# Kernel tuning notes

Hardware: AMD Instinct MI355X
Metric: run time of the kernel (lower is better)

## Reference

```python
import jax, jax.numpy as jnp
import numpy as np

EPS_BN = 1e-5
NEG = -9e15


def _bn_train(x, g, b):
    # x: [B, C, N]; training-mode BatchNorm1d with batch stats (biased var)
    m = jnp.mean(x, axis=(0, 2), keepdims=True)
    v = jnp.mean((x - m) ** 2, axis=(0, 2), keepdims=True)
    return (x - m) * jax.lax.rsqrt(v + EPS_BN) * g[None, :, None] + b[None, :, None]


def _conv1x1(w, x, b=None):
    # w: [O, C], x: [B, C, N] -> [B, O, N]
    y = jnp.einsum('oc,bcn->bon', w, x)
    if b is not None:
        y = y + b[None, :, None]
    return y


def _sa_layer(x, maskb, qk_w, v_w, v_b, t_w, t_b, bn_g, bn_b):
    # x: [B, C, N], maskb: [B, N] bool
    q = jnp.einsum('hc,bcn->bhn', qk_w, x)          # shared q/k weights
    energy = jnp.einsum('bhn,bhm->bnm', q, q)        # [B, N, N]
    pair = maskb[:, :, None] & maskb[:, None, :]
    energy = jnp.where(pair, energy, NEG)
    attn = jax.nn.softmax(energy, axis=-1)
    attn = attn / (1e-9 + jnp.sum(attn, axis=1, keepdims=True))  # L1 renorm over dim=1
    x_v = _conv1x1(v_w, x, v_b)                      # [B, C, N]
    x_r = jnp.einsum('bcn,bnm->bcm', x_v, attn)      # bmm(x_v, attention)
    t = _conv1x1(t_w, x - x_r, t_b)
    x_r = jax.nn.relu(_bn_train(t, bn_g, bn_b))
    return x + x_r


def setup_inputs() -> dict:
    key = jax.random.key(0)
    ks = jax.random.split(key, 16)
    B, C, N = 16, 256, 2048
    H = C // 4
    s = 0.05
    inp = {
        'x': jax.random.normal(ks[0], (B, C, N), jnp.float32),
        'mask': jax.random.randint(ks[1], (B, N), 0, 2, jnp.int32),
        'conv1_w': jax.random.normal(ks[2], (C, C), jnp.float32) * s,
        'conv2_w': jax.random.normal(ks[3], (C, C), jnp.float32) * s,
        'bn1_g': jnp.ones((C,), jnp.float32),
        'bn1_b': jnp.zeros((C,), jnp.float32),
        'bn2_g': jnp.ones((C,), jnp.float32),
        'bn2_b': jnp.zeros((C,), jnp.float32),
        'sa_qk_w': jax.random.normal(ks[4], (4, H, C), jnp.float32) * s,
        'sa_v_w': jax.random.normal(ks[5], (4, C, C), jnp.float32) * s,
        'sa_v_b': jax.random.normal(ks[6], (4, C), jnp.float32) * s,
        'sa_t_w': jax.random.normal(ks[7], (4, C, C), jnp.float32) * s,
        'sa_t_b': jax.random.normal(ks[8], (4, C), jnp.float32) * s,
        'sa_bn_g': jnp.ones((4, C), jnp.float32),
        'sa_bn_b': jnp.zeros((4, C), jnp.float32),
    }
    return inp


def reference(x, mask, conv1_w, conv2_w, bn1_g, bn1_b, bn2_g, bn2_b,
              sa_qk_w, sa_v_w, sa_v_b, sa_t_w, sa_t_b, sa_bn_g, sa_bn_b):
    maskb = mask.astype(bool)
    x = jax.nn.relu(_bn_train(_conv1x1(conv1_w, x), bn1_g, bn1_b))
    x = jax.nn.relu(_bn_train(_conv1x1(conv2_w, x), bn2_g, bn2_b))
    outs = []
    for i in range(4):
        x = _sa_layer(x, maskb, sa_qk_w[i], sa_v_w[i], sa_v_b[i],
                      sa_t_w[i], sa_t_b[i], sa_bn_g[i], sa_bn_b[i])
        outs.append(x)
    return jnp.concatenate(outs, axis=1)  # [B, 4C, N]
```

## Files before the change

kernel.cpp:

```cpp
#include <hip/hip_runtime.h>
#include <math.h>

#define BB 16
#define CC 256
#define NN 2048
#define HH 64
#define ATTSC 4096.0f
#define ATTINV (1.0f/4096.0f)
#define SQRTL2E 1.2011224087864498f
#define NEGB (-1.0e30f)
#define POSB (1.0e30f)

typedef _Float16 f16x8 __attribute__((ext_vector_type(8)));
typedef float f32x4 __attribute__((ext_vector_type(4)));

__device__ __forceinline__ f32x4 mfma16(f16x8 a, f16x8 b, f32x4 c) {
  return __builtin_amdgcn_mfma_f32_16x16x32_f16(a, b, c, 0, 0, 0);
}
__device__ __forceinline__ unsigned short f2h(float f) {
  _Float16 h = (_Float16)f;
  return __builtin_bit_cast(unsigned short, h);
}
__device__ __forceinline__ float h2f(unsigned short u) {
  return (float)__builtin_bit_cast(_Float16, u);
}
__device__ __forceinline__ unsigned pkrtz(float a, float b) {
  auto h = __builtin_amdgcn_cvt_pkrtz(a, b);
  return __builtin_bit_cast(unsigned, h);
}
__device__ __forceinline__ unsigned short* sp(unsigned short* base, int row, int colh) {
  return (unsigned short*)((char*)base + (row << 7) + (((colh << 1)) ^ ((row & 7) << 4)));
}
__device__ __forceinline__ const unsigned short* spc(const unsigned short* base, int row, int colh) {
  return (const unsigned short*)((const char*)base + (row << 7) + (((colh << 1)) ^ ((row & 7) << 4)));
}

__global__ __launch_bounds__(256)
void castw_kernel(const float* __restrict__ in, unsigned short* __restrict__ out,
                  int n, float scale)
{
  const int i = blockIdx.x*256 + threadIdx.x;
  if (i < n) out[i] = f2h(in[i]*scale);
}

__global__ __launch_bounds__(256)
void tcast_kernel(const float* __restrict__ src, long sstride,
                  unsigned short* __restrict__ dst)
{
  const int b = blockIdx.z, n0 = blockIdx.x*64, c0 = blockIdx.y*64;
  const int t = threadIdx.x;
  __shared__ float tile[64][66];
  const float* sb = src + (long)b*sstride;
  #pragma unroll
  for (int p = 0; p < 4; p++) {
    const int cr = (t>>4) + p*16;
    const int nq = (t&15)*4;
    const float4 v = *(const float4*)&sb[(long)(c0+cr)*NN + n0 + nq];
    tile[cr][nq+0] = v.x; tile[cr][nq+1] = v.y;
    tile[cr][nq+2] = v.z; tile[cr][nq+3] = v.w;
  }
  __syncthreads();
  unsigned short* db = dst + (long)b*NN*CC;
  #pragma unroll
  for (int p = 0; p < 4; p++) {
    const int nr = (t>>4) + p*16;
    const int cq = (t&15)*4;
    ushort4 o;
    o.x = f2h(tile[cq+0][nr]); o.y = f2h(tile[cq+1][nr]);
    o.z = f2h(tile[cq+2][nr]); o.w = f2h(tile[cq+3][nr]);
    *(ushort4*)&db[(long)(n0+nr)*CC + c0 + cq] = o;
  }
}

__global__ __launch_bounds__(256)
void gemm_xw_kernel(const unsigned short* __restrict__ A,
                    const unsigned short* __restrict__ W,
                    const float* __restrict__ bias,
                    unsigned short* __restrict__ out, int ocols)
{
  const int n0 = blockIdx.x*64, o0 = blockIdx.y*64, b = blockIdx.z;
  const int t = threadIdx.x;
  const int w = t >> 6, l = t & 63, lr = l & 15, lg = l >> 4;
  const int wr = w >> 1, wc = w & 1;
  __shared__ unsigned short Al[64][72];
  __shared__ unsigned short Bl[64][72];
  const unsigned short* Ab = A + ((long)b*NN + n0)*CC;
  const int srow = t >> 3, sg = t & 7;
  f32x4 acc[2][2];
  #pragma unroll
  for (int i = 0; i < 2; i++)
    #pragma unroll
    for (int j = 0; j < 2; j++) acc[i][j] = f32x4{0.f,0.f,0.f,0.f};

  for (int kt = 0; kt < 4; kt++) {
    const int k0 = kt*64;
    const uint4 a0 = *(const uint4*)&Ab[(long)srow*CC + k0 + sg*8];
    const uint4 a1 = *(const uint4*)&Ab[(long)(srow+32)*CC + k0 + sg*8];
    const uint4 w0 = *(const uint4*)&W[(long)(o0+srow)*CC + k0 + sg*8];
    const uint4 w1 = *(const uint4*)&W[(long)(o0+srow+32)*CC + k0 + sg*8];
    __syncthreads();
    *(uint4*)&Al[srow][sg*8] = a0;  *(uint4*)&Al[srow+32][sg*8] = a1;
    *(uint4*)&Bl[srow][sg*8] = w0;  *(uint4*)&Bl[srow+32][sg*8] = w1;
    __syncthreads();
    #pragma unroll
    for (int kf = 0; kf < 2; kf++) {
      f16x8 af0 = *(const f16x8*)&Al[wr*32 + lr]     [kf*32 + lg*8];
      f16x8 af1 = *(const f16x8*)&Al[wr*32 + 16 + lr][kf*32 + lg*8];
      f16x8 bf0 = *(const f16x8*)&Bl[wc*32 + lr]     [kf*32 + lg*8];
      f16x8 bf1 = *(const f16x8*)&Bl[wc*32 + 16 + lr][kf*32 + lg*8];
      acc[0][0] = mfma16(af0, bf0, acc[0][0]);
      acc[0][1] = mfma16(af0, bf1, acc[0][1]);
      acc[1][0] = mfma16(af1, bf0, acc[1][0]);
      acc[1][1] = mfma16(af1, bf1, acc[1][1]);
    }
  }
  #pragma unroll
  for (int j = 0; j < 2; j++) {
    const int oc = o0 + wc*32 + j*16 + lr;
    const float bo = bias ? bias[oc] : 0.f;
    #pragma unroll
    for (int i = 0; i < 2; i++) {
      const int nb = n0 + wr*32 + i*16 + lg*4;
      #pragma unroll
      for (int r = 0; r < 4; r++)
        out[((long)b*NN + nb + r)*ocols + oc] = f2h(acc[i][j][r] + bo);
    }
  }
}

__global__ __launch_bounds__(256)
void gemm_dxw_kernel(const unsigned short* __restrict__ X,
                     const unsigned short* __restrict__ XR,
                     const float* __restrict__ csumv,
                     const unsigned short* __restrict__ W,
                     const float* __restrict__ bias,
                     unsigned short* __restrict__ out)
{
  const int n0 = blockIdx.x*64, o0 = blockIdx.y*64, b = blockIdx.z;
  const int t = threadIdx.x;
  const int w = t >> 6, l = t & 63, lr = l & 15, lg = l >> 4;
  const int wr = w >> 1, wc = w & 1;
  __shared__ unsigned short Al[64][72];
  __shared__ unsigned short Bl[64][72];
  const unsigned short* Xb  = X  + ((long)b*NN + n0)*CC;
  const unsigned short* XRb = XR + ((long)b*NN + n0)*CC;
  const int srow = t >> 3, sg = t & 7;
  const long nrow0 = (long)b*NN + n0 + srow;
  const float inv0 = 1.f/(1e-9f + csumv[nrow0]);
  const float inv1 = 1.f/(1e-9f + csumv[nrow0+32]);
  f32x4 acc[2][2];
  #pragma unroll
  for (int i = 0; i < 2; i++)
    #pragma unroll
    for (int j = 0; j < 2; j++) acc[i][j] = f32x4{0.f,0.f,0.f,0.f};

  for (int kt = 0; kt < 4; kt++) {
    const int k0 = kt*64;
    const uint4 xa  = *(const uint4*)&Xb [(long)srow*CC + k0 + sg*8];
    const uint4 xra = *(const uint4*)&XRb[(long)srow*CC + k0 + sg*8];
    const uint4 xb_ = *(const uint4*)&Xb [(long)(srow+32)*CC + k0 + sg*8];
    const uint4 xrb = *(const uint4*)&XRb[(long)(srow+32)*CC + k0 + sg*8];
    const uint4 w0 = *(const uint4*)&W[(long)(o0+srow)*CC + k0 + sg*8];
    const uint4 w1 = *(const uint4*)&W[(long)(o0+srow+32)*CC + k0 + sg*8];
    uint4 da, db_;
    {
      const unsigned short* xs = (const unsigned short*)&xa;
      const unsigned short* rs = (const unsigned short*)&xra;
      unsigned short* ds = (unsigned short*)&da;
      #pragma unroll
      for (int j = 0; j < 8; j++) ds[j] = f2h(h2f(xs[j]) - h2f(rs[j])*inv0);
      xs = (const unsigned short*)&xb_;
      rs = (const unsigned short*)&xrb;
      ds = (unsigned short*)&db_;
      #pragma unroll
      for (int j = 0; j < 8; j++) ds[j] = f2h(h2f(xs[j]) - h2f(rs[j])*inv1);
    }
    __syncthreads();
    *(uint4*)&Al[srow][sg*8] = da;  *(uint4*)&Al[srow+32][sg*8] = db_;
    *(uint4*)&Bl[srow][sg*8] = w0;  *(uint4*)&Bl[srow+32][sg*8] = w1;
    __syncthreads();
    #pragma unroll
    for (int kf = 0; kf < 2; kf++) {
      f16x8 af0 = *(const f16x8*)&Al[wr*32 + lr]     [kf*32 + lg*8];
      f16x8 af1 = *(const f16x8*)&Al[wr*32 + 16 + lr][kf*32 + lg*8];
      f16x8 bf0 = *(const f16x8*)&Bl[wc*32 + lr]     [kf*32 + lg*8];
      f16x8 bf1 = *(const f16x8*)&Bl[wc*32 + 16 + lr][kf*32 + lg*8];
      acc[0][0] = mfma16(af0, bf0, acc[0][0]);
      acc[0][1] = mfma16(af0, bf1, acc[0][1]);
      acc[1][0] = mfma16(af1, bf0, acc[1][0]);
      acc[1][1] = mfma16(af1, bf1, acc[1][1]);
    }
  }
  #pragma unroll
  for (int j = 0; j < 2; j++) {
    const int oc = o0 + wc*32 + j*16 + lr;
    const float bo = bias[oc];
    #pragma unroll
    for (int i = 0; i < 2; i++) {
      const int nb = n0 + wr*32 + i*16 + lg*4;
      #pragma unroll
      for (int r = 0; r < 4; r++)
        out[((long)b*NN + nb + r)*CC + oc] = f2h(acc[i][j][r] + bo);
    }
  }
}

__global__ __launch_bounds__(256)
void gemm_wx_kernel(const unsigned short* __restrict__ W,
                    const unsigned short* __restrict__ X,
                    const float* __restrict__ bias,
                    unsigned short* __restrict__ out)
{
  const int n0 = blockIdx.x*64, o0 = blockIdx.y*64, b = blockIdx.z;
  const int t = threadIdx.x;
  const int w = t >> 6, l = t & 63, lr = l & 15, lg = l >> 4;
  const int wr = w >> 1, wc = w & 1;
  __shared__ unsigned short Al[64][72];
  __shared__ unsigned short Bl[64][72];
  const unsigned short* Xb = X + ((long)b*NN + n0)*CC;
  const int srow = t >> 3, sg = t & 7;
  f32x4 acc[2][2];
  #pragma unroll
  for (int i = 0; i < 2; i++)
    #pragma unroll
    for (int j = 0; j < 2; j++) acc[i][j] = f32x4{0.f,0.f,0.f,0.f};

  for (int kt = 0; kt < 4; kt++) {
    const int k0 = kt*64;
    const uint4 w0 = *(const uint4*)&W[(long)(o0+srow)*CC + k0 + sg*8];
    const uint4 w1 = *(const uint4*)&W[(long)(o0+srow+32)*CC + k0 + sg*8];
    const uint4 x0 = *(const uint4*)&Xb[(long)srow*CC + k0 + sg*8];
    const uint4 x1 = *(const uint4*)&Xb[(long)(srow+32)*CC + k0 + sg*8];
    __syncthreads();
    *(uint4*)&Al[srow][sg*8] = w0;  *(uint4*)&Al[srow+32][sg*8] = w1;
    *(uint4*)&Bl[srow][sg*8] = x0;  *(uint4*)&Bl[srow+32][sg*8] = x1;
    __syncthreads();
    #pragma unroll
    for (int kf = 0; kf < 2; kf++) {
      f16x8 af0 = *(const f16x8*)&Al[wr*32 + lr]     [kf*32 + lg*8];
      f16x8 af1 = *(const f16x8*)&Al[wr*32 + 16 + lr][kf*32 + lg*8];
      f16x8 bf0 = *(const f16x8*)&Bl[wc*32 + lr]     [kf*32 + lg*8];
      f16x8 bf1 = *(const f16x8*)&Bl[wc*32 + 16 + lr][kf*32 + lg*8];
      acc[0][0] = mfma16(af0, bf0, acc[0][0]);
      acc[0][1] = mfma16(af0, bf1, acc[0][1]);
      acc[1][0] = mfma16(af1, bf0, acc[1][0]);
      acc[1][1] = mfma16(af1, bf1, acc[1][1]);
    }
  }
  #pragma unroll
  for (int j = 0; j < 2; j++) {
    const int nc = n0 + wc*32 + j*16 + lr;
    #pragma unroll
    for (int i = 0; i < 2; i++) {
      #pragma unroll
      for (int r = 0; r < 4; r++) {
        const int oc = o0 + wr*32 + i*16 + lg*4 + r;
        out[((long)b*CC + oc)*NN + nc] = f2h(acc[i][j][r] + bias[oc]);
      }
    }
  }
}

__global__ __launch_bounds__(256)
void rowstat_kernel(const unsigned short* __restrict__ qT, const int* __restrict__ mask,
                    float* __restrict__ rmax, float* __restrict__ rinv)
{
  const int b = blockIdx.y, n0 = blockIdx.x*64;
  const int t = threadIdx.x, w = t>>6, l = t&63, lr = l&15, lg = l>>4;
  __shared__ unsigned short qs[64*64];
  __shared__ int ml[64];
  const int srow = t>>3, sg = t&7;
  const unsigned short* qbase = qT + (long)b*NN*HH;
  *(uint4*)sp(qs, srow,    sg*8) = *(const uint4*)&qbase[(long)(n0+srow)*HH + sg*8];
  *(uint4*)sp(qs, srow+32, sg*8) = *(const uint4*)&qbase[(long)(n0+srow+32)*HH + sg*8];
  int maskn[4];
  #pragma unroll
  for (int r = 0; r < 4; r++) maskn[r] = mask[(long)b*NN + n0 + w*16 + lg*4 + r];
  __syncthreads();
  f16x8 af0 = *(const f16x8*)spc(qs, w*16 + lr, lg*8);
  f16x8 af1 = *(const f16x8*)spc(qs, w*16 + lr, 32 + lg*8);
  float mx[4], sm[4];
  #pragma unroll
  for (int r = 0; r < 4; r++) { mx[r] = -INFINITY; sm[r] = 0.f; }

  for (int m0 = 0; m0 < NN; m0 += 64) {
    __syncthreads();
    *(uint4*)sp(qs, srow,    sg*8) = *(const uint4*)&qbase[(long)(m0+srow)*HH + sg*8];
    *(uint4*)sp(qs, srow+32, sg*8) = *(const uint4*)&qbase[(long)(m0+srow+32)*HH + sg*8];
    if (t < 64) ml[t] = mask[(long)b*NN + m0 + t];
    __syncthreads();
    float sv[4][4];
    #pragma unroll
    for (int tm = 0; tm < 4; tm++) {
      f32x4 s = f32x4{0.f,0.f,0.f,0.f};
      s = mfma16(af0, *(const f16x8*)spc(qs, tm*16 + lr, lg*8),      s);
      s = mfma16(af1, *(const f16x8*)spc(qs, tm*16 + lr, 32 + lg*8), s);
      const int cm = ml[tm*16 + lr];
      #pragma unroll
      for (int r = 0; r < 4; r++) sv[tm][r] = (maskn[r] && cm) ? s[r] : NEGB;
    }
    #pragma unroll
    for (int r = 0; r < 4; r++) {
      const float tmx = fmaxf(fmaxf(sv[0][r], sv[1][r]), fmaxf(sv[2][r], sv[3][r]));
      const float nm  = fmaxf(mx[r], tmx);
      sm[r] = sm[r]*exp2f(mx[r]-nm)
            + exp2f(sv[0][r]-nm) + exp2f(sv[1][r]-nm)
            + exp2f(sv[2][r]-nm) + exp2f(sv[3][r]-nm);
      mx[r] = nm;
    }
  }
  #pragma unroll
  for (int off = 1; off < 16; off <<= 1) {
    #pragma unroll
    for (int r = 0; r < 4; r++) {
      const float om = __shfl_xor(mx[r], off, 64);
      const float os = __shfl_xor(sm[r], off, 64);
      const float nm = fmaxf(mx[r], om);
      sm[r] = sm[r]*exp2f(mx[r]-nm) + os*exp2f(om-nm);
      mx[r] = nm;
    }
  }
  if (lr == 0) {
    #pragma unroll
    for (int r = 0; r < 4; r++) {
      const long idx = (long)b*NN + n0 + w*16 + lg*4 + r;
      rmax[idx] = maskn[r] ? mx[r] : POSB;
      rinv[idx] = 1.f/sm[r];
    }
  }
}

__global__ __launch_bounds__(256)
void yatt_kernel(const unsigned short* __restrict__ qT, const unsigned short* __restrict__ xv,
                 const int* __restrict__ mask, const float* __restrict__ rmax,
                 const float* __restrict__ rinv, unsigned short* __restrict__ xrTh,
                 float* __restrict__ csum)
{
  const int bid = blockIdx.x;
  const int swz = (bid & 7)*64 + (bid >> 3);
  const int b  = swz >> 5;
  const int m0 = (swz & 31) * 64;
  const int t = threadIdx.x, w = t>>6, l = t&63, lr = l&15, lg = l>>4;

  __shared__ unsigned short qm[64*64];
  __shared__ unsigned short qn[64*64];
  __shared__ unsigned short at[64*64];
  __shared__ float csred[4][4][16];

  const unsigned short* qbase = qT + (long)b*NN*HH;
  const unsigned short* xvb = xv + (long)b*CC*NN;
  const int srow = t>>3, sg = t&7;

  *(uint4*)sp(qm, srow,    sg*8) = *(const uint4*)&qbase[(long)(m0+srow)*HH + sg*8];
  *(uint4*)sp(qm, srow+32, sg*8) = *(const uint4*)&qbase[(long)(m0+srow+32)*HH + sg*8];
  float mcf[4];
  #pragma unroll
  for (int tm = 0; tm < 4; tm++)
    mcf[tm] = mask[(long)b*NN + m0 + tm*16 + lr] ? 1.f : 0.f;

  f32x4 acc[4][4];
  #pragma unroll
  for (int mi = 0; mi < 4; mi++)
    #pragma unroll
    for (int ci = 0; ci < 4; ci++) acc[mi][ci] = f32x4{0.f,0.f,0.f,0.f};
  float cs[4] = {0.f, 0.f, 0.f, 0.f};
  const int nb = w*16 + lg*4;

  for (int nc = 0; nc < NN; nc += 64) {
    __syncthreads();
    *(uint4*)sp(qn, srow,    sg*8) = *(const uint4*)&qbase[(long)(nc+srow)*HH + sg*8];
    *(uint4*)sp(qn, srow+32, sg*8) = *(const uint4*)&qbase[(long)(nc+srow+32)*HH + sg*8];
    const float4 rm4 = *(const float4*)&rmax[(long)b*NN + nc + nb];
    const float4 ri4 = *(const float4*)&rinv[(long)b*NN + nc + nb];
    const int4   mn4 = *(const int4*)&mask[(long)b*NN + nc + nb];
    f16x8 xb0[4], xb1[4];
    #pragma unroll
    for (int ci = 0; ci < 4; ci++) {
      const unsigned short* xp = &xvb[(long)(w*64 + ci*16 + lr)*NN + nc];
      xb0[ci] = *(const f16x8*)(xp + lg*8);
      xb1[ci] = *(const f16x8*)(xp + 32 + lg*8);
    }
    __syncthreads();
    const float rmv[4] = {rm4.x, rm4.y, rm4.z, rm4.w};
    const float rvs[4] = {ri4.x*ATTSC, ri4.y*ATTSC, ri4.z*ATTSC, ri4.w*ATTSC};
    const float dsc[4] = {mn4.x ? 0.f : rvs[0], mn4.y ? 0.f : rvs[1],
                          mn4.z ? 0.f : rvs[2], mn4.w ? 0.f : rvs[3]};
    const f16x8 a0 = *(const f16x8*)spc(qn, w*16 + lr, lg*8);
    const f16x8 a1 = *(const f16x8*)spc(qn, w*16 + lr, 32 + lg*8);
    #pragma unroll
    for (int tm = 0; tm < 4; tm++) {
      const f16x8 bq0 = *(const f16x8*)spc(qm, tm*16 + lr, lg*8);
      const f16x8 bq1 = *(const f16x8*)spc(qm, tm*16 + lr, 32 + lg*8);
      f32x4 s = mfma16(a0, bq0, f32x4{0.f,0.f,0.f,0.f});
      s = mfma16(a1, bq1, s);
      const float c0 = rvs[0]*mcf[tm], c1 = rvs[1]*mcf[tm];
      const float c2 = rvs[2]*mcf[tm], c3 = rvs[3]*mcf[tm];
      const float a0_ = exp2f(s[0]-rmv[0])*c0 + dsc[0];
      const float a1_ = exp2f(s[1]-rmv[1])*c1 + dsc[1];
      const float a2_ = exp2f(s[2]-rmv[2])*c2 + dsc[2];
      const float a3_ = exp2f(s[3]-rmv[3])*c3 + dsc[3];
      cs[tm] += (a0_ + a1_) + (a2_ + a3_);
      uint2 pk;
      pk.x = pkrtz(a0_, a1_);
      pk.y = pkrtz(a2_, a3_);
      *(uint2*)sp(at, tm*16 + lr, nb) = pk;
    }
    __syncthreads();
    #pragma unroll
    for (int mi = 0; mi < 4; mi++) {
      const f16x8 aa0 = *(const f16x8*)spc(at, mi*16 + lr, lg*8);
      const f16x8 aa1 = *(const f16x8*)spc(at, mi*16 + lr, 32 + lg*8);
      #pragma unroll
      for (int ci = 0; ci < 4; ci++) {
        acc[mi][ci] = mfma16(aa0, xb0[ci], acc[mi][ci]);
        acc[mi][ci] = mfma16(aa1, xb1[ci], acc[mi][ci]);
      }
    }
  }

  #pragma unroll
  for (int mi = 0; mi < 4; mi++)
    #pragma unroll
    for (int ci = 0; ci < 4; ci++)
      #pragma unroll
      for (int r = 0; r < 4; r++)
        xrTh[((long)b*NN + m0 + mi*16 + lg*4 + r)*CC + w*64 + ci*16 + lr] =
            f2h(acc[mi][ci][r] * ATTINV);

  #pragma unroll
  for (int tm = 0; tm < 4; tm++) {
    cs[tm] += __shfl_xor(cs[tm], 16, 64);
    cs[tm] += __shfl_xor(cs[tm], 32, 64);
    if (lg == 0) csred[tm][w][lr] = cs[tm];
  }
  __syncthreads();
  if (t < 64) {
    const int tm = t >> 4, mr = t & 15;
    const float v = csred[tm][0][mr] + csred[tm][1][mr]
                  + csred[tm][2][mr] + csred[tm][3][mr];
    csum[(long)b*NN + m0 + tm*16 + mr] = v * ATTINV;
  }
}

__global__ __launch_bounds__(256)
void bnstatsA_kernel(const unsigned short* __restrict__ tTh, float* __restrict__ part)
{
  const int k = blockIdx.x;
  const int c = threadIdx.x;
  float s = 0.f, sq = 0.f;
  const long r0 = (long)k*128;
  for (int r = 0; r < 128; r++) {
    const float v = h2f(tTh[(r0 + r)*CC + c]);
    s += v; sq += v*v;
  }
  part[(long)k*CC + c] = s;
  part[(long)(256 + k)*CC + c] = sq;
}

__global__ __launch_bounds__(1024)
void bnstatsB_kernel(const float* __restrict__ part,
                     float* __restrict__ mean, float* __restrict__ istd)
{
  const int t = threadIdx.x, c = t & 255, q = t >> 8;
  float s = 0.f, sq = 0.f;
  for (int k = q*64; k < q*64 + 64; k++) {
    s  += part[(long)k*CC + c];
    sq += part[(long)(256 + k)*CC + c];
  }
  __shared__ float ls[4][256], lq[4][256];
  ls[q][c] = s; lq[q][c] = sq;
  __syncthreads();
  if (q == 0) {
    s  = ls[0][c] + ls[1][c] + ls[2][c] + ls[3][c];
    sq = lq[0][c] + lq[1][c] + lq[2][c] + lq[3][c];
    const float mu = s / (float)(BB*NN);
    mean[c] = mu;
    istd[c] = rsqrtf(sq/(float)(BB*NN) - mu*mu + 1e-5f);
  }
}

__global__ __launch_bounds__(256)
void bnapplyA_kernel(const unsigned short* __restrict__ tTh, const float* __restrict__ mean,
                     const float* __restrict__ istd, const float* __restrict__ g,
                     const float* __restrict__ bt, unsigned short* __restrict__ xTo)
{
  __shared__ float sc[CC], sh[CC];
  const int t = threadIdx.x;
  {
    const float is = istd[t], gg = g[t];
    sc[t] = is*gg; sh[t] = bt[t] - mean[t]*is*gg;
  }
  __syncthreads();
  const long i = (long)blockIdx.x*256 + t;
  const long base = i*8;
  const int c8 = (int)(base & 255);
  const uint4 v = *(const uint4*)&tTh[base];
  const unsigned short* hs = (const unsigned short*)&v;
  uint4 ou;
  unsigned short* os = (unsigned short*)&ou;
  #pragma unroll
  for (int j = 0; j < 8; j++)
    os[j] = f2h(fmaxf(h2f(hs[j])*sc[c8+j] + sh[c8+j], 0.f));
  *(uint4*)&xTo[base] = ou;
}

__global__ __launch_bounds__(256)
void bnfuse_kernel(const unsigned short* __restrict__ tTh, const float* __restrict__ mean,
                   const float* __restrict__ istd, const float* __restrict__ g,
                   const float* __restrict__ bt, const float* __restrict__ resid,
                   long rstride, float* __restrict__ outp, long ostride,
                   unsigned short* __restrict__ xtn)
{
  const int b = blockIdx.z, n0 = blockIdx.x*64, c0 = blockIdx.y*64;
  const int t = threadIdx.x;
  __shared__ float tile[64][66];
  const unsigned short* tb_ = tTh + ((long)b*NN + n0)*CC;
  const int cq = (t&15)*4;
  float scv[4], shv[4];
  #pragma unroll
  for (int j = 0; j < 4; j++) {
    const int c = c0 + cq + j;
    const float is = istd[c], gg = g[c];
    scv[j] = is*gg; shv[j] = bt[c] - mean[c]*is*gg;
  }
  #pragma unroll
  for (int p = 0; p < 4; p++) {
    const int nr = (t>>4) + p*16;
    const ushort4 v = *(const ushort4*)&tb_[(long)nr*CC + c0 + cq];
    tile[cq+0][nr] = fmaxf(h2f(v.x)*scv[0] + shv[0], 0.f);
    tile[cq+1][nr] = fmaxf(h2f(v.y)*scv[1] + shv[1], 0.f);
    tile[cq+2][nr] = fmaxf(h2f(v.z)*scv[2] + shv[2], 0.f);
    tile[cq+3][nr] = fmaxf(h2f(v.w)*scv[3] + shv[3], 0.f);
  }
  __syncthreads();
  const int nq = (t&15)*4;
  #pragma unroll
  for (int p = 0; p < 4; p++) {
    const int cr = (t>>4) + p*16;
    float4 o;
    o.x = tile[cr][nq+0]; o.y = tile[cr][nq+1];
    o.z = tile[cr][nq+2]; o.w = tile[cr][nq+3];
    if (resid) {
      const float4 rv = *(const float4*)&resid[(long)b*rstride + (long)(c0+cr)*NN + n0 + nq];
      o.x += rv.x; o.y += rv.y; o.z += rv.z; o.w += rv.w;
    }
    *(float4*)&outp[(long)b*ostride + (long)(c0+cr)*NN + n0 + nq] = o;
    tile[cr][nq+0] = o.x; tile[cr][nq+1] = o.y;
    tile[cr][nq+2] = o.z; tile[cr][nq+3] = o.w;
  }
  if (xtn) {
    __syncthreads();
    #pragma unroll
    for (int p = 0; p < 4; p++) {
      const int nr = (t>>4) + p*16;
      ushort4 o;
      o.x = f2h(tile[cq+0][nr]); o.y = f2h(tile[cq+1][nr]);
      o.z = f2h(tile[cq+2][nr]); o.w = f2h(tile[cq+3][nr]);
      *(ushort4*)&xtn[((long)b*NN + n0+nr)*CC + c0 + cq] = o;
    }
  }
}

extern "C" void kernel_launch(void* const* d_in, const int* in_sizes, int n_in,
                              void* d_out, int out_size, void* d_ws, size_t ws_size,
                              hipStream_t stream)
{
  const float* x_in   = (const float*)d_in[0];
  const int*   mask   = (const int*)d_in[1];
  const float* conv1w = (const float*)d_in[2];
  const float* conv2w = (const float*)d_in[3];
  const float* bn1g   = (const float*)d_in[4];
  const float* bn1b   = (const float*)d_in[5];
  const float* bn2g   = (const float*)d_in[6];
  const float* bn2b   = (const float*)d_in[7];
  const float* qkw    = (const float*)d_in[8];
  const float* vw     = (const float*)d_in[9];
  const float* vb     = (const float*)d_in[10];
  const float* tw     = (const float*)d_in[11];
  const float* tb     = (const float*)d_in[12];
  const float* bng    = (const float*)d_in[13];
  const float* bnb    = (const float*)d_in[14];
  float* out = (float*)d_out;

  const long BCN = (long)BB*CC*NN;
  const long CN  = (long)CC*NN;
  const long BN  = (long)BB*NN;
  char* p = (char*)d_ws;
  unsigned short* xTa  = (unsigned short*)p; p += BCN*2;
  unsigned short* xTb  = (unsigned short*)p; p += BCN*2;
  unsigned short* qTb  = (unsigned short*)p; p += (long)BB*NN*HH*2;
  unsigned short* xvb  = (unsigned short*)p; p += BCN*2;
  unsigned short* tTh  = (unsigned short*)p; p += BCN*2;
  unsigned short* xrTh = (unsigned short*)p; p += BCN*2;
  float* xbuf  = (float*)p; p += BCN*4;
  float* rmaxb = (float*)p; p += BN*4;
  float* rinvb = (float*)p; p += BN*4;
  float* csumb = (float*)p; p += BN*4;
  float* partb = (float*)p; p += 512L*CC*4;
  float* meanb = (float*)p; p += CC*4;
  float* istdb = (float*)p; p += CC*4;
  unsigned short* wc1 = (unsigned short*)p; p += (long)CC*CC*2;
  unsigned short* wc2 = (unsigned short*)p; p += (long)CC*CC*2;
  unsigned short* wqk = (unsigned short*)p; p += 4L*HH*CC*2;
  unsigned short* wv  = (unsigned short*)p; p += 4L*CC*CC*2;
  unsigned short* wt  = (unsigned short*)p; p += 4L*CC*CC*2;

  const dim3 gT(NN/64, CC/64, BB);
  const dim3 gQ(NN/64, 1, BB);
  const dim3 gRS(NN/64, BB);
  const dim3 blk(256);

  castw_kernel<<<dim3(256), blk, 0, stream>>>(conv1w, wc1, CC*CC, 1.f);
  castw_kernel<<<dim3(256), blk, 0, stream>>>(conv2w, wc2, CC*CC, 1.f);
  castw_kernel<<<dim3(256), blk, 0, stream>>>(qkw, wqk, 4*HH*CC, SQRTL2E);
  castw_kernel<<<dim3(1024), blk, 0, stream>>>(vw, wv, 4*CC*CC, 1.f);
  castw_kernel<<<dim3(1024), blk, 0, stream>>>(tw, wt, 4*CC*CC, 1.f);

  tcast_kernel<<<gT, blk, 0, stream>>>(x_in, CN, xTa);
  gemm_xw_kernel<<<gT, blk, 0, stream>>>(xTa, wc1, nullptr, tTh, CC);
  bnstatsA_kernel<<<dim3(256), blk, 0, stream>>>(tTh, partb);
  bnstatsB_kernel<<<dim3(1), dim3(1024), 0, stream>>>(partb, meanb, istdb);
  bnapplyA_kernel<<<dim3(4096), blk, 0, stream>>>(tTh, meanb, istdb, bn1g, bn1b, xTb);
  gemm_xw_kernel<<<gT, blk, 0, stream>>>(xTb, wc2, nullptr, tTh, CC);
  bnstatsA_kernel<<<dim3(256), blk, 0, stream>>>(tTh, partb);
  bnstatsB_kernel<<<dim3(1), dim3(1024), 0, stream>>>(partb, meanb, istdb);
  bnfuse_kernel<<<gT, blk, 0, stream>>>(tTh, meanb, istdb, bn2g, bn2b,
                                        nullptr, 0, xbuf, CN, xTa);

  unsigned short* cur = xTa;
  unsigned short* nxt = xTb;
  for (int i = 0; i < 4; i++) {
    gemm_xw_kernel<<<gQ, blk, 0, stream>>>(cur, wqk + (long)i*HH*CC, nullptr, qTb, HH);
    rowstat_kernel<<<gRS, blk, 0, stream>>>(qTb, mask, rmaxb, rinvb);
    gemm_wx_kernel<<<gT, blk, 0, stream>>>(wv + (long)i*CC*CC, cur, vb + (long)i*CC, xvb);
    yatt_kernel<<<dim3(512), blk, 0, stream>>>(qTb, xvb, mask, rmaxb, rinvb, xrTh, csumb);
    gemm_dxw_kernel<<<gT, blk, 0, stream>>>(cur, xrTh, csumb,
                                            wt + (long)i*CC*CC, tb + (long)i*CC, tTh);
    bnstatsA_kernel<<<dim3(256), blk, 0, stream>>>(tTh, partb);
    bnstatsB_kernel<<<dim3(1), dim3(1024), 0, stream>>>(partb, meanb, istdb);
    const float* resid = (i == 0) ? xbuf : (out + (long)(i-1)*CN);
    const long rstr = (i == 0) ? CN : 4*CN;
    bnfuse_kernel<<<gT, blk, 0, stream>>>(tTh, meanb, istdb,
                                          bng + (long)i*CC, bnb + (long)i*CC,
                                          resid, rstr, out + (long)i*CN, 4*CN,
                                          (i < 3) ? nxt : nullptr);
    unsigned short* tmp = cur; cur = nxt; nxt = tmp;
  }

  (void)in_sizes; (void)n_in; (void)out_size; (void)ws_size;
}
```

Baseline: 802.4 us.

## Widen attention kernel to 512 threads and 128-wide key chunks

The fused attention-times-values kernel now runs with 8 waves per block and processes 128 key columns per iteration instead of 64. Each wave covers 32 output channels instead of 64, which halves its accumulator registers, and the number of loop iterations and barriers is halved. The attention tile in shared memory doubles to 128 columns with a new swizzle helper. The goal is more waves in flight for latency hiding and fewer barriers, at the cost of more shared memory per block and redundant exp computation per 128-column chunk.

```diff
diff --git a/kernel.cpp b/kernel.cpp
--- a/kernel.cpp
+++ b/kernel.cpp
@@ -33,6 +33,12 @@
 }
 __device__ __forceinline__ const unsigned short* spc(const unsigned short* base, int row, int colh) {
   return (const unsigned short*)((const char*)base + (row << 7) + (((colh << 1)) ^ ((row & 7) << 4)));
+}
+__device__ __forceinline__ unsigned short* sp2(unsigned short* base, int row, int colh) {
+  return (unsigned short*)((char*)base + (row << 8) + (((colh << 1)) ^ ((row & 7) << 4)));
+}
+__device__ __forceinline__ const unsigned short* spc2(const unsigned short* base, int row, int colh) {
+  return (const unsigned short*)((const char*)base + (row << 8) + (((colh << 1)) ^ ((row & 7) << 4)));
 }
 
 __global__ __launch_bounds__(256)
@@ -330,7 +336,7 @@
   }
 }
 
-__global__ __launch_bounds__(256)
+__global__ __launch_bounds__(512)
 void yatt_kernel(const unsigned short* __restrict__ qT, const unsigned short* __restrict__ xv,
                  const int* __restrict__ mask, const float* __restrict__ rmax,
                  const float* __restrict__ rinv, unsigned short* __restrict__ xrTh,
@@ -343,42 +349,42 @@
   const int t = threadIdx.x, w = t>>6, l = t&63, lr = l&15, lg = l>>4;
 
   __shared__ unsigned short qm[64*64];
-  __shared__ unsigned short qn[64*64];
-  __shared__ unsigned short at[64*64];
-  __shared__ float csred[4][4][16];
+  __shared__ unsigned short qn[128*64];
+  __shared__ unsigned short at[64*128];
+  __shared__ float csred[4][8][16];
 
   const unsigned short* qbase = qT + (long)b*NN*HH;
   const unsigned short* xvb = xv + (long)b*CC*NN;
   const int srow = t>>3, sg = t&7;
 
-  *(uint4*)sp(qm, srow,    sg*8) = *(const uint4*)&qbase[(long)(m0+srow)*HH + sg*8];
-  *(uint4*)sp(qm, srow+32, sg*8) = *(const uint4*)&qbase[(long)(m0+srow+32)*HH + sg*8];
+  *(uint4*)sp(qm, srow, sg*8) = *(const uint4*)&qbase[(long)(m0+srow)*HH + sg*8];
   float mcf[4];
   #pragma unroll
   for (int tm = 0; tm < 4; tm++)
     mcf[tm] = mask[(long)b*NN + m0 + tm*16 + lr] ? 1.f : 0.f;
 
-  f32x4 acc[4][4];
+  f32x4 acc[4][2];
   #pragma unroll
   for (int mi = 0; mi < 4; mi++)
     #pragma unroll
-    for (int ci = 0; ci < 4; ci++) acc[mi][ci] = f32x4{0.f,0.f,0.f,0.f};
+    for (int ci = 0; ci < 2; ci++) acc[mi][ci] = f32x4{0.f,0.f,0.f,0.f};
   float cs[4] = {0.f, 0.f, 0.f, 0.f};
   const int nb = w*16 + lg*4;
 
-  for (int nc = 0; nc < NN; nc += 64) {
+  for (int nc = 0; nc < NN; nc += 128) {
     __syncthreads();
     *(uint4*)sp(qn, srow,    sg*8) = *(const uint4*)&qbase[(long)(nc+srow)*HH + sg*8];
-    *(uint4*)sp(qn, srow+32, sg*8) = *(const uint4*)&qbase[(long)(nc+srow+32)*HH + sg*8];
+    *(uint4*)sp(qn, srow+64, sg*8) = *(const uint4*)&qbase[(long)(nc+srow+64)*HH + sg*8];
     const float4 rm4 = *(const float4*)&rmax[(long)b*NN + nc + nb];
     const float4 ri4 = *(const float4*)&rinv[(long)b*NN + nc + nb];
     const int4   mn4 = *(const int4*)&mask[(long)b*NN + nc + nb];
-    f16x8 xb0[4], xb1[4];
-    #pragma unroll
-    for (int ci = 0; ci < 4; ci++) {
-      const unsigned short* xp = &xvb[(long)(w*64 + ci*16 + lr)*NN + nc];
-      xb0[ci] = *(const f16x8*)(xp + lg*8);
-      xb1[ci] = *(const f16x8*)(xp + 32 + lg*8);
+    f16x8 xb[2][4];
+    #pragma unroll
+    for (int ci = 0; ci < 2; ci++) {
+      const unsigned short* xp = &xvb[(long)(w*32 + ci*16 + lr)*NN + nc];
+      #pragma unroll
+      for (int ks = 0; ks < 4; ks++)
+        xb[ci][ks] = *(const f16x8*)(xp + ks*32 + lg*8);
     }
     __syncthreads();
     const float rmv[4] = {rm4.x, rm4.y, rm4.z, rm4.w};
@@ -403,17 +409,16 @@
       uint2 pk;
       pk.x = pkrtz(a0_, a1_);
       pk.y = pkrtz(a2_, a3_);
-      *(uint2*)sp(at, tm*16 + lr, nb) = pk;
+      *(uint2*)sp2(at, tm*16 + lr, nb) = pk;
     }
     __syncthreads();
     #pragma unroll
     for (int mi = 0; mi < 4; mi++) {
-      const f16x8 aa0 = *(const f16x8*)spc(at, mi*16 + lr, lg*8);
-      const f16x8 aa1 = *(const f16x8*)spc(at, mi*16 + lr, 32 + lg*8);
-      #pragma unroll
-      for (int ci = 0; ci < 4; ci++) {
-        acc[mi][ci] = mfma16(aa0, xb0[ci], acc[mi][ci]);
-        acc[mi][ci] = mfma16(aa1, xb1[ci], acc[mi][ci]);
+      #pragma unroll
+      for (int ks = 0; ks < 4; ks++) {
+        const f16x8 aa = *(const f16x8*)spc2(at, mi*16 + lr, ks*32 + lg*8);
+        acc[mi][0] = mfma16(aa, xb[0][ks], acc[mi][0]);
+        acc[mi][1] = mfma16(aa, xb[1][ks], acc[mi][1]);
       }
     }
   }
@@ -421,10 +426,10 @@
   #pragma unroll
   for (int mi = 0; mi < 4; mi++)
     #pragma unroll
-    for (int ci = 0; ci < 4; ci++)
+    for (int ci = 0; ci < 2; ci++)
       #pragma unroll
       for (int r = 0; r < 4; r++)
-        xrTh[((long)b*NN + m0 + mi*16 + lg*4 + r)*CC + w*64 + ci*16 + lr] =
+        xrTh[((long)b*NN + m0 + mi*16 + lg*4 + r)*CC + w*32 + ci*16 + lr] =
             f2h(acc[mi][ci][r] * ATTINV);
 
   #pragma unroll
@@ -436,8 +441,9 @@
   __syncthreads();
   if (t < 64) {
     const int tm = t >> 4, mr = t & 15;
-    const float v = csred[tm][0][mr] + csred[tm][1][mr]
-                  + csred[tm][2][mr] + csred[tm][3][mr];
+    float v = 0.f;
+    #pragma unroll
+    for (int w2 = 0; w2 < 8; w2++) v += csred[tm][w2][mr];
     csum[(long)b*NN + m0 + tm*16 + mr] = v * ATTINV;
   }
 }
@@ -633,7 +639,7 @@
     gemm_xw_kernel<<<gQ, blk, 0, stream>>>(cur, wqk + (long)i*HH*CC, nullptr, qTb, HH);
     rowstat_kernel<<<gRS, blk, 0, stream>>>(qTb, mask, rmaxb, rinvb);
     gemm_wx_kernel<<<gT, blk, 0, stream>>>(wv + (long)i*CC*CC, cur, vb + (long)i*CC, xvb);
-    yatt_kernel<<<dim3(512), blk, 0, stream>>>(qTb, xvb, mask, rmaxb, rinvb, xrTh, csumb);
+    yatt_kernel<<<dim3(512), dim3(512), 0, stream>>>(qTb, xvb, mask, rmaxb, rinvb, xrTh, csumb);
     gemm_dxw_kernel<<<gT, blk, 0, stream>>>(cur, xrTh, csumb,
                                             wt + (long)i*CC*CC, tb + (long)i*CC, tTh);
     bnstatsA_kernel<<<dim3(256), blk, 0, stream>>>(tTh, partb);
```

Result: slower. 953.4 us (+18.8%).
